# Optimization experiments

Hardware: AMD Instinct MI355X
Metric: run time of the kernel (lower is better)

Reference implementation:

```python
import jax, jax.numpy as jnp
import numpy as np

P = 7       # patch (window) size
H_HEADS = 8
D_HEAD = 64
SCALE = D_HEAD ** -0.5


def setup_inputs() -> dict:
    key = jax.random.key(0)
    k1, k2, k3, k4 = jax.random.split(key, 4)
    dim, inner = 256, H_HEADS * D_HEAD
    fmap = jax.random.normal(k1, (32, 56, 56, dim), dtype=jnp.float32)
    Wq = jax.random.normal(k2, (dim, inner), dtype=jnp.float32) * (dim ** -0.5)
    Wkv = jax.random.normal(k3, (dim, 2 * inner), dtype=jnp.float32) * (dim ** -0.5)
    Wo = jax.random.normal(k4, (inner, dim), dtype=jnp.float32) * (inner ** -0.5)
    bo = jnp.zeros((dim,), dtype=jnp.float32)
    return {"fmap": fmap, "Wq": Wq, "Wkv": Wkv, "Wo": Wo, "bo": bo}


def reference(fmap, Wq, Wkv, Wo, bo):
    b, X, Y, c = fmap.shape
    x, y = X // P, Y // P
    h, d = H_HEADS, D_HEAD
    # window partition: b (x p1) (y p2) c -> (b x y) p1 p2 c
    f = fmap.reshape(b, x, P, y, P, c).transpose(0, 1, 3, 2, 4, 5)
    f = f.reshape(b * x * y, P, P, c)
    # 1x1 convs == matmul over channels
    q = f @ Wq                       # (B, p, p, h*d)
    k_, v = jnp.split(f @ Wkv, 2, axis=-1)
    B = b * x * y
    pp = P * P
    def to_heads(t):  # (B,p,p,h*d) -> (B,h,pp,d)
        return t.reshape(B, pp, h, d).transpose(0, 2, 1, 3)
    q, k_, v = map(to_heads, (q, k_, v))
    dots = jnp.einsum('bhid,bhjd->bhij', q, k_) * SCALE
    attn = jax.nn.softmax(dots, axis=-1)
    out = jnp.einsum('bhij,bhjd->bhid', attn, v)      # (B,h,pp,d)
    # (b x y h) (p1 p2) d -> b (x p1) (y p2) (h d)
    out = out.reshape(b, x, y, h, P, P, d)
    out = out.transpose(0, 1, 4, 2, 5, 3, 6).reshape(b, X, Y, h * d)
    return out @ Wo + bo
```

## Files before the change

kernel.cpp:

```cpp
#include <hip/hip_runtime.h>
#include <hip/hip_bf16.h>

typedef __bf16 bf16;
typedef __bf16 bf16x4 __attribute__((ext_vector_type(4)));
typedef __bf16 bf16x8 __attribute__((ext_vector_type(8)));
typedef float f32x4 __attribute__((ext_vector_type(4)));

#define TOK 100352
#define ATT_SCALE 0.125f

#define GLOAD_LDS16(g, l)                                                        \
  __builtin_amdgcn_global_load_lds((const __attribute__((address_space(1))) void*)(g), \
                                   (__attribute__((address_space(3))) void*)(l), 16, 0, 0)

__global__ __launch_bounds__(256) void transpose_cast_k(const float* __restrict__ in,
                                                        bf16* __restrict__ out, int R, int C) {
  __shared__ float t[32][33];
  int c0 = blockIdx.x * 32, r0 = blockIdx.y * 32;
  int tx = threadIdx.x, ty = threadIdx.y;
#pragma unroll
  for (int i = ty; i < 32; i += 8)
    t[i][tx] = in[(size_t)(r0 + i) * C + c0 + tx];
  __syncthreads();
#pragma unroll
  for (int i = ty; i < 32; i += 8)
    out[(size_t)(c0 + i) * R + r0 + tx] = (bf16)t[tx][i];
}

__global__ __launch_bounds__(256) void qkvg_k(const float* __restrict__ fmap,
                                              const bf16* __restrict__ Bt,
                                              bf16* __restrict__ qkv2,
                                              bf16* __restrict__ Vtg, int wbase0) {
  __shared__ bf16 Bs[2][128 * 64];
  const int tid = threadIdx.x;
  const int lane = tid & 63, wv = tid >> 6;
  const int l15 = lane & 15, l4 = lane >> 4;
  const int g = blockIdx.x;
  const int blk = blockIdx.y;
  bf16x8 af[2][8];
  int wl[2], tt[2];
#pragma unroll
  for (int m = 0; m < 2; ++m) {
    int tokl = blk * 128 + wv * 32 + m * 16 + l15;
    int w = tokl / 49, t = tokl - w * 49;
    wl[m] = w; tt[m] = t;
    int wg = wbase0 + w;
    int p1 = t / 7, p2 = t - p1 * 7;
    const float* ab = fmap +
        (size_t)((((wg >> 6) * 56) + ((wg >> 3) & 7) * 7 + p1) * 56 + (wg & 7) * 7 + p2) * 256;
#pragma unroll
    for (int j = 0; j < 8; ++j) {
      const float* p = ab + j * 32 + l4 * 8;
      float4 f0 = *(const float4*)p;
      float4 f1 = *(const float4*)(p + 4);
      bf16x8 o;
      o[0] = (bf16)f0.x; o[1] = (bf16)f0.y; o[2] = (bf16)f0.z; o[3] = (bf16)f0.w;
      o[4] = (bf16)f1.x; o[5] = (bf16)f1.y; o[6] = (bf16)f1.z; o[7] = (bf16)f1.w;
      af[m][j] = o;
    }
  }
  const int sg = lane >> 3;
  const int scol = ((lane & 7) ^ (sg & 7)) * 8;
#define STAGE_B(tt_, buf_)                                                                   \
  do {                                                                                       \
    int bn_ = g * 4 + ((tt_) >> 2), ks_ = (tt_) & 3;                                         \
    _Pragma("unroll") for (int i_ = 0; i_ < 4; ++i_)                                         \
        GLOAD_LDS16(Bt + (size_t)(bn_ * 128 + wv * 32 + i_ * 8 + sg) * 256 + ks_ * 64 + scol,\
                    Bs[buf_] + wv * 2048 + i_ * 512);                                        \
  } while (0)

  f32x4 acc[2][8] = {};
  STAGE_B(0, 0);
  __syncthreads();
#pragma unroll
  for (int t = 0; t < 16; ++t) {
    const int cur = t & 1, ks = t & 3;
    if (t < 15) STAGE_B(t + 1, cur ^ 1);
#pragma unroll
    for (int kk = 0; kk < 2; ++kk) {
      bf16x8 bfr[8];
#pragma unroll
      for (int n = 0; n < 8; ++n) {
        int rv = n * 16 + l15;
        bfr[n] = *(const bf16x8*)((const char*)Bs[cur] +
                 ((rv * 128 + kk * 64 + l4 * 16) ^ ((rv & 7) << 4)));
      }
#pragma unroll
      for (int m = 0; m < 2; ++m)
#pragma unroll
        for (int n = 0; n < 8; ++n)
          acc[m][n] = __builtin_amdgcn_mfma_f32_16x16x32_bf16(bfr[n], af[m][ks * 2 + kk],
                                                              acc[m][n], 0, 0, 0);
    }
    if (ks == 3) {
      const int bn = g * 4 + (t >> 2);
      if (g < 2) {
#pragma unroll
        for (int m = 0; m < 2; ++m) {
          size_t row = (size_t)blk * 128 + wv * 32 + m * 16 + l15;
#pragma unroll
          for (int n = 0; n < 8; ++n) {
            bf16x4 pk;
#pragma unroll
            for (int r = 0; r < 4; ++r) pk[r] = (bf16)acc[m][n][r];
            *(bf16x4*)(qkv2 + row * 1024 + bn * 128 + n * 16 + l4 * 4) = pk;
          }
        }
      } else {
#pragma unroll
        for (int m = 0; m < 2; ++m) {
#pragma unroll
          for (int n = 0; n < 8; ++n) {
            int d0 = (bn - 8) * 128 + n * 16 + l4 * 4;
            int h = d0 >> 6, dd = d0 & 63;
            size_t vb = ((size_t)wl[m] * 8 + h) * 4096 + (size_t)dd * 64 + tt[m];
#pragma unroll
            for (int r = 0; r < 4; ++r) Vtg[vb + (size_t)r * 64] = (bf16)acc[m][n][r];
          }
        }
      }
#pragma unroll
      for (int m = 0; m < 2; ++m)
#pragma unroll
        for (int n = 0; n < 8; ++n) acc[m][n] = (f32x4){0.f, 0.f, 0.f, 0.f};
    }
    __syncthreads();
  }
#undef STAGE_B
}

__global__ __launch_bounds__(256) void attn2_k(const bf16* __restrict__ qkv2,
                                               const bf16* __restrict__ Vtg,
                                               const bf16* __restrict__ Wo_t,
                                               const float* __restrict__ bias,
                                               float* __restrict__ out, int wbase) {
  __shared__ bf16 Qs[64 * 64], Ks[64 * 64], Vt[64 * 64], Ps[4 * 16 * 64], HO[64 * 64];
  const int w = blockIdx.x;
  const int tid = threadIdx.x, lane = tid & 63, wv = tid >> 6;
  const int l15 = lane & 15, l4 = lane >> 4;
  const size_t bqk = (size_t)w * 49 * 1024;
  const bf16* vbase = Vtg + (size_t)w * 8 * 4096;
  const int wg = wbase + w;
  char* pbase = (char*)Ps + wv * 2048;
  const int sr = wv * 8 + (lane >> 3);
  const int scc = ((lane & 7) ^ ((lane >> 3) & 7)) * 8;
  f32x4 acco[4][4] = {};
  for (int h = 0; h < 8; ++h) {
#pragma unroll
    for (int i = 0; i < 2; ++i) {
      GLOAD_LDS16(qkv2 + bqk + (size_t)(i * 32 + sr) * 1024 + h * 64 + scc,
                  Qs + i * 2048 + wv * 512);
      GLOAD_LDS16(qkv2 + bqk + (size_t)(i * 32 + sr) * 1024 + 512 + h * 64 + scc,
                  Ks + i * 2048 + wv * 512);
      GLOAD_LDS16(vbase + (size_t)h * 4096 + (i * 32 + sr) * 64 + scc,
                  Vt + i * 2048 + wv * 512);
    }
    __syncthreads();
    f32x4 s[4] = {};
#pragma unroll
    for (int kk = 0; kk < 2; ++kk) {
      int rq = wv * 16 + l15;
      bf16x8 aq = *(const bf16x8*)((const char*)Qs +
                  ((rq * 128 + kk * 64 + l4 * 16) ^ ((rq & 7) << 4)));
#pragma unroll
      for (int n = 0; n < 4; ++n) {
        int rk = n * 16 + l15;
        bf16x8 bk = *(const bf16x8*)((const char*)Ks +
                    ((rk * 128 + kk * 64 + l4 * 16) ^ ((rk & 7) << 4)));
        s[n] = __builtin_amdgcn_mfma_f32_16x16x32_bf16(aq, bk, s[n], 0, 0, 0);
      }
    }
    float pr[4][4];
#pragma unroll
    for (int reg = 0; reg < 4; ++reg) {
      float m = -1e30f;
#pragma unroll
      for (int n = 0; n < 4; ++n) {
        float v = s[n][reg] * ATT_SCALE;
        if (n * 16 + l15 < 49) m = fmaxf(m, v);
      }
#pragma unroll
      for (int d = 1; d < 16; d <<= 1) m = fmaxf(m, __shfl_xor(m, d));
      float sum = 0.f;
#pragma unroll
      for (int n = 0; n < 4; ++n) {
        float p = (n * 16 + l15 < 49) ? __expf(s[n][reg] * ATT_SCALE - m) : 0.f;
        pr[n][reg] = p;
        sum += p;
      }
#pragma unroll
      for (int d = 1; d < 16; d <<= 1) sum += __shfl_xor(sum, d);
      float inv = 1.f / sum;
#pragma unroll
      for (int n = 0; n < 4; ++n) pr[n][reg] *= inv;
    }
#pragma unroll
    for (int n = 0; n < 4; ++n)
#pragma unroll
      for (int reg = 0; reg < 4; ++reg) {
        int rl = l4 * 4 + reg, col = n * 16 + l15;
        int off = ((rl * 64 + col) * 2) ^ ((rl & 7) << 4);
        *(bf16*)(pbase + off) = (bf16)pr[n][reg];
      }
    f32x4 o[4] = {};
#pragma unroll
    for (int kk = 0; kk < 2; ++kk) {
      int rp = l15;
      bf16x8 ap = *(const bf16x8*)(pbase +
                  ((rp * 128 + kk * 64 + l4 * 16) ^ ((rp & 7) << 4)));
#pragma unroll
      for (int n = 0; n < 4; ++n) {
        int rv = n * 16 + l15;
        bf16x8 bv = *(const bf16x8*)((const char*)Vt +
                    ((rv * 128 + kk * 64 + l4 * 16) ^ ((rv & 7) << 4)));
        o[n] = __builtin_amdgcn_mfma_f32_16x16x32_bf16(bv, ap, o[n], 0, 0, 0);
      }
    }
    {
      int hrow = wv * 16 + l15;
#pragma unroll
      for (int n = 0; n < 4; ++n) {
        bf16x4 pk;
#pragma unroll
        for (int r = 0; r < 4; ++r) pk[r] = (bf16)o[n][r];
        int off = (hrow * 128 + n * 32 + l4 * 8) ^ ((hrow & 7) << 4);
        *(bf16x4*)((char*)HO + off) = pk;
      }
    }
    __syncthreads();
#pragma unroll
    for (int kk = 0; kk < 2; ++kk) {
      bf16x8 af[4];
#pragma unroll
      for (int m = 0; m < 4; ++m) {
        int r = m * 16 + l15;
        af[m] = *(const bf16x8*)((const char*)HO +
                 ((r * 128 + kk * 64 + l4 * 16) ^ ((r & 7) << 4)));
      }
#pragma unroll
      for (int n = 0; n < 4; ++n) {
        int wr = wv * 64 + n * 16 + l15;
        bf16x8 bv = *(const bf16x8*)(Wo_t + (size_t)wr * 512 + h * 64 + kk * 32 + l4 * 8);
#pragma unroll
        for (int m = 0; m < 4; ++m)
          acco[m][n] = __builtin_amdgcn_mfma_f32_16x16x32_bf16(bv, af[m], acco[m][n], 0, 0, 0);
      }
    }
  }
  int bb = wg >> 6, xx = (wg >> 3) & 7, yy = wg & 7;
#pragma unroll
  for (int m = 0; m < 4; ++m) {
    int rl = m * 16 + l15;
    if (rl < 49) {
      int p1 = rl / 7, p2 = rl - p1 * 7;
      size_t orow = (size_t)(bb * 56 + xx * 7 + p1) * 56 + yy * 7 + p2;
      float* op = out + orow * 256 + wv * 64;
#pragma unroll
      for (int n = 0; n < 4; ++n) {
        int col = n * 16 + l4 * 4;
        float4 b4 = *(const float4*)(bias + wv * 64 + col);
        float4 v;
        v.x = acco[m][n][0] + b4.x;
        v.y = acco[m][n][1] + b4.y;
        v.z = acco[m][n][2] + b4.z;
        v.w = acco[m][n][3] + b4.w;
        *(float4*)(op + col) = v;
      }
    }
  }
}

extern "C" void kernel_launch(void* const* d_in, const int* in_sizes, int n_in,
                              void* d_out, int out_size, void* d_ws, size_t ws_size,
                              hipStream_t stream) {
  const float* fmap = (const float*)d_in[0];
  const float* Wq = (const float*)d_in[1];
  const float* Wkv = (const float*)d_in[2];
  const float* Wo = (const float*)d_in[3];
  const float* bo = (const float*)d_in[4];
  float* out = (float*)d_out;
  char* ws = (char*)d_ws;

  const size_t WQKV_B = 1536ull * 256 * 2;
  const size_t WO_B = 256ull * 512 * 2;
  const size_t wbytes = WQKV_B + WO_B;

  int nc = 0;
  size_t Tc = 0, VtgB = 0;
  for (int c = 2; c <= 16; c <<= 1) {
    size_t tc = TOK / c;
    size_t vb = (tc / 49) * 65536ull;
    if (wbytes + vb + tc * 2048ull + 65536ull <= ws_size) { nc = c; Tc = tc; VtgB = vb; break; }
  }
  if (nc == 0) return;

  bf16* Wqkv_t = (bf16*)(ws);
  bf16* Wo_t = (bf16*)(ws + WQKV_B);
  bf16* Vtg = (bf16*)(ws + wbytes);
  bf16* qkv2 = (bf16*)(ws + wbytes + VtgB);

  hipMemsetAsync(Vtg, 0, VtgB, stream);

  hipLaunchKernelGGL(transpose_cast_k, dim3(16, 8), dim3(32, 8), 0, stream, Wq, Wqkv_t, 256, 512);
  hipLaunchKernelGGL(transpose_cast_k, dim3(32, 8), dim3(32, 8), 0, stream, Wkv,
                     Wqkv_t + 512 * 256, 256, 1024);
  hipLaunchKernelGGL(transpose_cast_k, dim3(8, 16), dim3(32, 8), 0, stream, Wo, Wo_t, 512, 256);

  for (int c = 0; c < nc; ++c) {
    int tok0 = (int)(c * Tc);
    int wloc = (int)(Tc / 49);
    hipLaunchKernelGGL(qkvg_k, dim3(3, (int)(Tc / 128)), dim3(256), 0, stream, fmap, Wqkv_t,
                       qkv2, Vtg, tok0 / 49);
    hipLaunchKernelGGL(attn2_k, dim3(wloc), dim3(256), 0, stream, qkv2, Vtg, Wo_t, bo, out,
                       tok0 / 49);
  }
}
```

Baseline: 344.4 us.

## Pre-pack Wo into MFMA fragment order, merge weight prep, widen QKV blocks

Wo is now packed into a layout that matches the MFMA B-fragments, so each lane in the attention kernel does one contiguous 16-byte load instead of strided row loads. The Wq/Wkv transpose launches are merged into one kernel. The QKV projection kernel moves to 512 threads per block covering 256 tokens, so each staged weight tile in LDS is shared by twice as many tokens. The chunk-count search is capped at 8. The larger blocks raise per-block register and LDS pressure and halve the number of blocks.

Result: slower. 352.6 us (+2.4%).

```diff
diff --git a/kernel.cpp b/kernel.cpp
--- a/kernel.cpp
+++ b/kernel.cpp
@@ -13,10 +13,16 @@
   __builtin_amdgcn_global_load_lds((const __attribute__((address_space(1))) void*)(g), \
                                    (__attribute__((address_space(3))) void*)(l), 16, 0, 0)
 
-__global__ __launch_bounds__(256) void transpose_cast_k(const float* __restrict__ in,
-                                                        bf16* __restrict__ out, int R, int C) {
+__global__ __launch_bounds__(256) void wprep_k(const float* __restrict__ Wq,
+                                               const float* __restrict__ Wkv,
+                                               bf16* __restrict__ Wqkv_t) {
   __shared__ float t[32][33];
-  int c0 = blockIdx.x * 32, r0 = blockIdx.y * 32;
+  int bx = blockIdx.x;
+  const float* in;
+  bf16* out;
+  int C, c0, r0 = blockIdx.y * 32;
+  if (bx < 16) { in = Wq; C = 512; c0 = bx * 32; out = Wqkv_t; }
+  else { in = Wkv; C = 1024; c0 = (bx - 16) * 32; out = Wqkv_t + 512 * 256; }
   int tx = threadIdx.x, ty = threadIdx.y;
 #pragma unroll
   for (int i = ty; i < 32; i += 8)
@@ -24,10 +30,23 @@
   __syncthreads();
 #pragma unroll
   for (int i = ty; i < 32; i += 8)
-    out[(size_t)(c0 + i) * R + r0 + tx] = (bf16)t[tx][i];
-}
-
-__global__ __launch_bounds__(256) void qkvg_k(const float* __restrict__ fmap,
+    out[(size_t)(c0 + i) * 256 + r0 + tx] = (bf16)t[tx][i];
+}
+
+__global__ __launch_bounds__(256) void pack_wo_k(const float* __restrict__ Wo,
+                                                 bf16* __restrict__ P) {
+  int t = blockIdx.x * 256 + threadIdx.x;
+  int f = t >> 6, l = t & 63;
+  int kk = f & 1, h = (f >> 1) & 7, n = (f >> 4) & 3, wvv = f >> 6;
+  int row = wvv * 64 + n * 16 + (l & 15);
+  int col = h * 64 + kk * 32 + (l >> 4) * 8;
+  bf16x8 o;
+#pragma unroll
+  for (int e = 0; e < 8; ++e) o[e] = (bf16)Wo[(size_t)(col + e) * 256 + row];
+  *(bf16x8*)(P + (size_t)f * 512 + l * 8) = o;
+}
+
+__global__ __launch_bounds__(512) void qkvg_k(const float* __restrict__ fmap,
                                               const bf16* __restrict__ Bt,
                                               bf16* __restrict__ qkv2,
                                               bf16* __restrict__ Vtg, int wbase0) {
@@ -41,7 +60,7 @@
   int wl[2], tt[2];
 #pragma unroll
   for (int m = 0; m < 2; ++m) {
-    int tokl = blk * 128 + wv * 32 + m * 16 + l15;
+    int tokl = blk * 256 + wv * 32 + m * 16 + l15;
     int w = tokl / 49, t = tokl - w * 49;
     wl[m] = w; tt[m] = t;
     int wg = wbase0 + w;
@@ -64,9 +83,9 @@
 #define STAGE_B(tt_, buf_)                                                                   \
   do {                                                                                       \
     int bn_ = g * 4 + ((tt_) >> 2), ks_ = (tt_) & 3;                                         \
-    _Pragma("unroll") for (int i_ = 0; i_ < 4; ++i_)                                         \
-        GLOAD_LDS16(Bt + (size_t)(bn_ * 128 + wv * 32 + i_ * 8 + sg) * 256 + ks_ * 64 + scol,\
-                    Bs[buf_] + wv * 2048 + i_ * 512);                                        \
+    _Pragma("unroll") for (int i_ = 0; i_ < 2; ++i_)                                         \
+        GLOAD_LDS16(Bt + (size_t)(bn_ * 128 + wv * 16 + i_ * 8 + sg) * 256 + ks_ * 64 + scol,\
+                    Bs[buf_] + (wv * 2 + i_) * 512 + lane * 8);                              \
   } while (0)
 
   f32x4 acc[2][8] = {};
@@ -97,7 +116,7 @@
       if (g < 2) {
 #pragma unroll
         for (int m = 0; m < 2; ++m) {
-          size_t row = (size_t)blk * 128 + wv * 32 + m * 16 + l15;
+          size_t row = (size_t)blk * 256 + wv * 32 + m * 16 + l15;
 #pragma unroll
           for (int n = 0; n < 8; ++n) {
             bf16x4 pk;
@@ -131,7 +150,7 @@
 
 __global__ __launch_bounds__(256) void attn2_k(const bf16* __restrict__ qkv2,
                                                const bf16* __restrict__ Vtg,
-                                               const bf16* __restrict__ Wo_t,
+                                               const bf16* __restrict__ Wo_p,
                                                const float* __restrict__ bias,
                                                float* __restrict__ out, int wbase) {
   __shared__ bf16 Qs[64 * 64], Ks[64 * 64], Vt[64 * 64], Ps[4 * 16 * 64], HO[64 * 64];
@@ -239,8 +258,8 @@
       }
 #pragma unroll
       for (int n = 0; n < 4; ++n) {
-        int wr = wv * 64 + n * 16 + l15;
-        bf16x8 bv = *(const bf16x8*)(Wo_t + (size_t)wr * 512 + h * 64 + kk * 32 + l4 * 8);
+        int f = ((wv * 4 + n) * 8 + h) * 2 + kk;
+        bf16x8 bv = *(const bf16x8*)(Wo_p + (size_t)f * 512 + lane * 8);
 #pragma unroll
         for (int m = 0; m < 4; ++m)
           acco[m][n] = __builtin_amdgcn_mfma_f32_16x16x32_bf16(bv, af[m], acco[m][n], 0, 0, 0);
@@ -282,12 +301,12 @@
   char* ws = (char*)d_ws;
 
   const size_t WQKV_B = 1536ull * 256 * 2;
-  const size_t WO_B = 256ull * 512 * 2;
-  const size_t wbytes = WQKV_B + WO_B;
+  const size_t WOP_B = 256ull * 512 * 2;
+  const size_t wbytes = WQKV_B + WOP_B;
 
   int nc = 0;
   size_t Tc = 0, VtgB = 0;
-  for (int c = 2; c <= 16; c <<= 1) {
+  for (int c = 2; c <= 8; c <<= 1) {
     size_t tc = TOK / c;
     size_t vb = (tc / 49) * 65536ull;
     if (wbytes + vb + tc * 2048ull + 65536ull <= ws_size) { nc = c; Tc = tc; VtgB = vb; break; }
@@ -295,23 +314,21 @@
   if (nc == 0) return;
 
   bf16* Wqkv_t = (bf16*)(ws);
-  bf16* Wo_t = (bf16*)(ws + WQKV_B);
+  bf16* Wo_p = (bf16*)(ws + WQKV_B);
   bf16* Vtg = (bf16*)(ws + wbytes);
   bf16* qkv2 = (bf16*)(ws + wbytes + VtgB);
 
   hipMemsetAsync(Vtg, 0, VtgB, stream);
 
-  hipLaunchKernelGGL(transpose_cast_k, dim3(16, 8), dim3(32, 8), 0, stream, Wq, Wqkv_t, 256, 512);
-  hipLaunchKernelGGL(transpose_cast_k, dim3(32, 8), dim3(32, 8), 0, stream, Wkv,
-                     Wqkv_t + 512 * 256, 256, 1024);
-  hipLaunchKernelGGL(transpose_cast_k, dim3(8, 16), dim3(32, 8), 0, stream, Wo, Wo_t, 512, 256);
+  hipLaunchKernelGGL(wprep_k, dim3(48, 8), dim3(32, 8), 0, stream, Wq, Wkv, Wqkv_t);
+  hipLaunchKernelGGL(pack_wo_k, dim3(64), dim3(256), 0, stream, Wo, Wo_p);
 
   for (int c = 0; c < nc; ++c) {
     int tok0 = (int)(c * Tc);
     int wloc = (int)(Tc / 49);
-    hipLaunchKernelGGL(qkvg_k, dim3(3, (int)(Tc / 128)), dim3(256), 0, stream, fmap, Wqkv_t,
+    hipLaunchKernelGGL(qkvg_k, dim3(3, (int)(Tc / 256)), dim3(512), 0, stream, fmap, Wqkv_t,
                        qkv2, Vtg, tok0 / 49);
-    hipLaunchKernelGGL(attn2_k, dim3(wloc), dim3(256), 0, stream, qkv2, Vtg, Wo_t, bo, out,
+    hipLaunchKernelGGL(attn2_k, dim3(wloc), dim3(256), 0, stream, qkv2, Vtg, Wo_p, bo, out,
                        tok0 / 49);
   }
 }
```
